# Performance work log

Measured on AMD Instinct MI355X. Metric: run time of the kernel, lower is better.

The kernel has to match this reference:

```python
import jax, jax.numpy as jnp
import numpy as np

B, C, H, W = 16, 256, 32, 32
NUM_LAYERS = 30
OUT = 16  # sqrt(out_channels)
EPS = 1e-5


def setup_inputs() -> dict:
    key = jax.random.key(0)
    k1, k2, k3 = jax.random.split(key, 3)
    x = jax.random.normal(k1, (B, C, H, W), dtype=jnp.float32)
    # delta_t ~ small positive values (module inits ~N(0.01, 0.005))
    delta_t = jax.random.uniform(k2, (NUM_LAYERS, 1), dtype=jnp.float32) * 0.02
    matrices = jax.random.normal(k3, (NUM_LAYERS, 1, 1, OUT, OUT), dtype=jnp.float32) * 0.1
    gamma = jnp.ones((H * W,), dtype=jnp.float32)   # BatchNorm2d weight, oc = i*i = H*W
    beta = jnp.zeros((H * W,), dtype=jnp.float32)   # BatchNorm2d bias
    return {"x": x, "delta_t": delta_t, "matrices": matrices, "gamma": gamma, "beta": beta}


def _bn_relu6(z, gamma, beta):
    # training-mode BatchNorm2d over channel axis 1 (channels = H*W), then ReLU6
    mean = jnp.mean(z, axis=(0, 2, 3), keepdims=True)
    var = jnp.mean(jnp.square(z - mean), axis=(0, 2, 3), keepdims=True)  # biased var
    zhat = (z - mean) * jax.lax.rsqrt(var + EPS)
    g = gamma.reshape(1, -1, 1, 1)
    b = beta.reshape(1, -1, 1, 1)
    return jnp.clip(zhat * g + b, 0.0, 6.0)


def reference(x, delta_t, matrices, gamma, beta):
    b, c, h, w = x.shape
    hw = h * w
    # feature_reshape: [B,C,H,W] -> [B,HW,C] -> [B,HW,out,out] (inn == out branch)
    x1 = x.reshape(b, c, hw).transpose(0, 2, 1).reshape(b, hw, OUT, OUT)
    dt = jnp.clip(delta_t, 0.0, 6.0)[:, 0]  # relu6(delta_t), shape [L]

    def step(y0, params):
        m, dtl = params  # m: [1,1,out,out] broadcasts elementwise against x1
        dydt = -y0 + _bn_relu6(y0 + m * x1, gamma, beta)
        return y0 + dtl * dydt, None

    y0, _ = jax.lax.scan(step, x1, (matrices, dt))
    # (y0 + x1): [B, HW, out, out] -> view [B,H,W,out*out] -> permute to [B,out*out,H,W]
    y = (y0 + x1).reshape(b, h, w, OUT * OUT).transpose(0, 3, 1, 2)
    return y
```

## Files before the change

kernel.cpp:

```cpp
#include <hip/hip_runtime.h>

typedef float v2f __attribute__((ext_vector_type(2)));
typedef float v4f __attribute__((ext_vector_type(4)));

#define HW      1024
#define NROWS   4096
#define NLAYERS 30
#define TPB     256

static __device__ __forceinline__ v2f pk_fma(v2f a, v2f b, v2f c) {
    v2f d; asm("v_pk_fma_f32 %0, %1, %2, %3" : "=v"(d) : "v"(a), "v"(b), "v"(c));
    return d;
}
static __device__ __forceinline__ v2f pk_add(v2f a, v2f b) {
    v2f d; asm("v_pk_add_f32 %0, %1, %2" : "=v"(d) : "v"(a), "v"(b));
    return d;
}
static __device__ __forceinline__ v2f pk_mul(v2f a, v2f b) {
    v2f d; asm("v_pk_mul_f32 %0, %1, %2" : "=v"(d) : "v"(a), "v"(b));
    return d;
}

template <int CTRL, int RMASK>
__device__ __forceinline__ float dpp_add(float x) {
    int t = __builtin_amdgcn_update_dpp(0, __builtin_bit_cast(int, x),
                                        CTRL, RMASK, 0xf, true);
    return x + __builtin_bit_cast(float, t);
}
__device__ __forceinline__ float wave_sum64(float x) {
    x = dpp_add<0x111, 0xf>(x);
    x = dpp_add<0x112, 0xf>(x);
    x = dpp_add<0x114, 0xf>(x);
    x = dpp_add<0x118, 0xf>(x);
    x = dpp_add<0x142, 0xa>(x);
    x = dpp_add<0x143, 0xc>(x);
    return x;
}
__device__ __forceinline__ float bcast63(float x) {
    return __builtin_bit_cast(float,
        __builtin_amdgcn_readlane(__builtin_bit_cast(int, x), 63));
}

__global__ __launch_bounds__(TPB) void txp64(const float* __restrict__ src,
                                             float* __restrict__ dst,
                                             int M, int N) {
    __shared__ float tile[64][65];
    const int n0 = blockIdx.x * 64;
    const int m0 = blockIdx.y * 64;
    const int tx = threadIdx.x & 63;
    const int ty = threadIdx.x >> 6;
#pragma unroll
    for (int i = 0; i < 16; ++i) {
        const int r = ty + 4 * i;
        tile[r][tx] = src[(size_t)(m0 + r) * N + n0 + tx];
    }
    __syncthreads();
#pragma unroll
    for (int i = 0; i < 16; ++i) {
        const int r = ty + 4 * i;
        dst[(size_t)(n0 + r) * M + m0 + tx] = tile[tx][r];
    }
}

__global__ __launch_bounds__(64, 1) void ode_zrec(
    float* ws, const float* __restrict__ delta_t,
    const float* __restrict__ matrices, const float* __restrict__ gamma,
    const float* __restrict__ beta) {

    const int p    = blockIdx.x;
    const int lane = threadIdx.x;
    const int c0   = 4 * lane;
    float* row = ws + (size_t)p * NROWS;

    __shared__ float xs[NROWS];

    const float gp = gamma[p];
    const float bp = beta[p];

    v2f z[32];
    v2f s0 = {0.f, 0.f}, s1 = {0.f, 0.f}, q0 = {0.f, 0.f}, q1 = {0.f, 0.f};

    {
        const v4f m4 = *(const v4f*)(matrices + c0);
        const v2f mA = {m4.x, m4.y}, mB = {m4.z, m4.w};
#pragma unroll
        for (int j = 0; j < 16; ++j) {
            const v4f x4 = *(const v4f*)(row + 4 * lane + 256 * j);
            *(v4f*)&xs[4 * lane + 256 * j] = x4;
            const v2f xA = {x4.x, x4.y}, xB = {x4.z, x4.w};
            z[2 * j]     = pk_fma(mA, xA, xA);
            z[2 * j + 1] = pk_fma(mB, xB, xB);
            s0 = pk_add(s0, z[2 * j]);
            q0 = pk_fma(z[2 * j], z[2 * j], q0);
            s1 = pk_add(s1, z[2 * j + 1]);
            q1 = pk_fma(z[2 * j + 1], z[2 * j + 1], q1);
        }
    }

    v4f   mqc = *(const v4f*)(matrices + c0);
    v4f   mqn = *(const v4f*)(matrices + 256 + c0);
    float dtc = delta_t[0];
    float dtn = delta_t[1];

    for (int k = 0; k < NLAYERS - 1; ++k) {
        const int k2 = (k + 2 < NLAYERS) ? k + 2 : NLAYERS - 1;
        const v4f   mq2   = *(const v4f*)(matrices + k2 * 256 + c0);
        const float dt_nn = delta_t[k2];

        const v2f sv = pk_add(s0, s1);
        const v2f qv = pk_add(q0, q1);
        const float S = bcast63(wave_sum64(sv.x + sv.y));
        const float Q = bcast63(wave_sum64(qv.x + qv.y));

        const float dtk  = __builtin_amdgcn_fmed3f(dtc, 0.0f, 6.0f);
        const float mean = S * (1.0f / 4096.0f);
        const float var  = fmaf(-mean, mean, Q * (1.0f / 4096.0f));
        const float rstd = rsqrtf(var + 1e-5f);
        const float g    = gp * rstd;
        const float b    = fmaf(-mean, g, bp);
        const float om   = 1.0f - dtk;
        const v2f g2 = {g, g}, b2 = {b, b};
        const v2f dt2 = {dtk, dtk};
        const v2f om2 = {om, om};
        const v2f omn = {-om, -om};
        const v2f mcA = {mqc.x, mqc.y}, mcB = {mqc.z, mqc.w};
        const v2f mnA = {mqn.x, mqn.y}, mnB = {mqn.z, mqn.w};
        const v2f dmA = pk_fma(omn, mcA, mnA);
        const v2f dmB = pk_fma(omn, mcB, mnB);

        s0 = (v2f){0.f, 0.f}; s1 = (v2f){0.f, 0.f};
        q0 = (v2f){0.f, 0.f}; q1 = (v2f){0.f, 0.f};

#pragma unroll
        for (int j = 0; j < 16; ++j) {
            const v4f x4 = *(const v4f*)&xs[4 * lane + 256 * j];
            const v2f xA = {x4.x, x4.y}, xB = {x4.z, x4.w};
            {
                const int e = 2 * j;
                v2f a = pk_fma(z[e], g2, b2);
                a.x = __builtin_amdgcn_fmed3f(a.x, 0.0f, 6.0f);
                a.y = __builtin_amdgcn_fmed3f(a.y, 0.0f, 6.0f);
                v2f t = pk_mul(dt2, a);
                t = pk_fma(dmA, xA, t);
                z[e] = pk_fma(om2, z[e], t);
                s0 = pk_add(s0, z[e]);
                q0 = pk_fma(z[e], z[e], q0);
            }
            {
                const int e = 2 * j + 1;
                v2f a = pk_fma(z[e], g2, b2);
                a.x = __builtin_amdgcn_fmed3f(a.x, 0.0f, 6.0f);
                a.y = __builtin_amdgcn_fmed3f(a.y, 0.0f, 6.0f);
                v2f t = pk_mul(dt2, a);
                t = pk_fma(dmB, xB, t);
                z[e] = pk_fma(om2, z[e], t);
                s1 = pk_add(s1, z[e]);
                q1 = pk_fma(z[e], z[e], q1);
            }
        }

        mqc = mqn; mqn = mq2; dtc = dtn; dtn = dt_nn;
    }

    {
        const v2f sv = pk_add(s0, s1);
        const v2f qv = pk_add(q0, q1);
        const float S = bcast63(wave_sum64(sv.x + sv.y));
        const float Q = bcast63(wave_sum64(qv.x + qv.y));

        const float dtk  = __builtin_amdgcn_fmed3f(dtc, 0.0f, 6.0f);
        const float mean = S * (1.0f / 4096.0f);
        const float var  = fmaf(-mean, mean, Q * (1.0f / 4096.0f));
        const float rstd = rsqrtf(var + 1e-5f);
        const float g    = gp * rstd;
        const float b    = fmaf(-mean, g, bp);
        const float om   = 1.0f - dtk;
        const v2f g2 = {g, g}, b2 = {b, b};
        const v2f dt2 = {dtk, dtk};
        const v2f om2 = {om, om};
        const v2f omn = {-om, -om};
        const v2f one2 = {1.0f, 1.0f};
        const v2f mcA = {mqc.x, mqc.y}, mcB = {mqc.z, mqc.w};
        const v2f dmA = pk_fma(omn, mcA, one2);
        const v2f dmB = pk_fma(omn, mcB, one2);

#pragma unroll
        for (int j = 0; j < 16; ++j) {
            const v4f x4 = *(const v4f*)&xs[4 * lane + 256 * j];
            const v2f xA = {x4.x, x4.y}, xB = {x4.z, x4.w};
            v2f o0, o1;
            {
                const int e = 2 * j;
                v2f a = pk_fma(z[e], g2, b2);
                a.x = __builtin_amdgcn_fmed3f(a.x, 0.0f, 6.0f);
                a.y = __builtin_amdgcn_fmed3f(a.y, 0.0f, 6.0f);
                v2f t = pk_mul(dt2, a);
                t = pk_fma(dmA, xA, t);
                o0 = pk_fma(om2, z[e], t);
            }
            {
                const int e = 2 * j + 1;
                v2f a = pk_fma(z[e], g2, b2);
                a.x = __builtin_amdgcn_fmed3f(a.x, 0.0f, 6.0f);
                a.y = __builtin_amdgcn_fmed3f(a.y, 0.0f, 6.0f);
                v2f t = pk_mul(dt2, a);
                t = pk_fma(dmB, xB, t);
                o1 = pk_fma(om2, z[e], t);
            }
            v4f o4; o4.x = o0.x; o4.y = o0.y; o4.z = o1.x; o4.w = o1.y;
            *(v4f*)(row + 4 * lane + 256 * j) = o4;
        }
    }
}

__global__ __launch_bounds__(TPB) void ode_fused(const float* __restrict__ x,
                                                 const float* __restrict__ delta_t,
                                                 const float* __restrict__ matrices,
                                                 const float* __restrict__ gamma,
                                                 const float* __restrict__ beta,
                                                 float* __restrict__ out) {
    const int bid = blockIdx.x;
    const int p   = ((bid & 7) << 7) | (bid >> 3);
    const int t   = threadIdx.x;

    __shared__ float smat[(NLAYERS + 1) * 256];
    __shared__ float sdt[NLAYERS];
    __shared__ __align__(16) v2f red[2][4];

#pragma unroll
    for (int i = 0; i < NLAYERS; ++i)
        smat[i * 256 + t] = matrices[i * 256 + t];
    if (t < NLAYERS)
        sdt[t] = __builtin_amdgcn_fmed3f(delta_t[t], 0.0f, 6.0f);

    v2f x1[8], y[8];
#pragma unroll
    for (int k = 0; k < 8; ++k) {
        x1[k].x = x[(size_t)(t + 512 * k) * HW + p];
        x1[k].y = x[(size_t)(t + 512 * k + 256) * HW + p];
        y[k] = x1[k];
    }

    const float gp   = gamma[p];
    const float bp   = beta[p];
    const int   wid  = t >> 6;
    const int   lane = t & 63;

    __syncthreads();
    float m_cur = smat[t];

    for (int l = 0; l < NLAYERS; ++l) {
        const float dtl = sdt[l];
        const v2f m2    = {m_cur, m_cur};
        const v2f dt2   = {dtl, dtl};
        const v2f om2   = {1.0f - dtl, 1.0f - dtl};

        v2f z[8];
        v2f sA = {0.f, 0.f}, sB = {0.f, 0.f};
        v2f qA = {0.f, 0.f}, qB = {0.f, 0.f};
#pragma unroll
        for (int k = 0; k < 8; k += 2) {
            z[k]     = __builtin_elementwise_fma(m2, x1[k], y[k]);
            z[k + 1] = __builtin_elementwise_fma(m2, x1[k + 1], y[k + 1]);
            sA += z[k];
            sB += z[k + 1];
            qA = __builtin_elementwise_fma(z[k], z[k], qA);
            qB = __builtin_elementwise_fma(z[k + 1], z[k + 1], qB);
        }
#pragma unroll
        for (int k = 0; k < 8; ++k) y[k] *= om2;

        const v2f sv = sA + sB;
        const v2f qv = qA + qB;
        float s = wave_sum64(sv.x + sv.y);
        float q = wave_sum64(qv.x + qv.y);

        const int par = l & 1;
        if (lane == 63) { v2f w; w.x = s; w.y = q; red[par][wid] = w; }
        m_cur = smat[(l + 1) * 256 + t];
        __syncthreads();

        const float4 r0 = *(const float4*)&red[par][0];
        const float4 r1 = *(const float4*)&red[par][2];
        const float S  = (r0.x + r0.z) + (r1.x + r1.z);
        const float S2 = (r0.y + r0.w) + (r1.y + r1.w);

        const float mean = S * (1.0f / 4096.0f);
        const float var  = fmaf(-mean, mean, S2 * (1.0f / 4096.0f));
        const float rstd = rsqrtf(var + 1e-5f);
        const float g    = gp * rstd;
        const float bb   = fmaf(-mean, g, bp);
        const v2f g2 = {g, g}, b2 = {bb, bb};
        const v2f z0 = {0.f, 0.f}, s6 = {6.f, 6.f};
#pragma unroll
        for (int k = 0; k < 8; ++k) {
            v2f a = __builtin_elementwise_fma(z[k], g2, b2);
            a = __builtin_elementwise_max(a, z0);
            a = __builtin_elementwise_min(a, s6);
            y[k] = __builtin_elementwise_fma(dt2, a, y[k]);
        }
    }

#pragma unroll
    for (int k = 0; k < 8; ++k) {
        out[(size_t)(t + 512 * k) * HW + p]       = y[k].x + x1[k].x;
        out[(size_t)(t + 512 * k + 256) * HW + p] = y[k].y + x1[k].y;
    }
}

extern "C" void kernel_launch(void* const* d_in, const int* in_sizes, int n_in,
                              void* d_out, int out_size, void* d_ws, size_t ws_size,
                              hipStream_t stream) {
    const float* x        = (const float*)d_in[0];
    const float* delta_t  = (const float*)d_in[1];
    const float* matrices = (const float*)d_in[2];
    const float* gamma    = (const float*)d_in[3];
    const float* beta     = (const float*)d_in[4];
    float* out = (float*)d_out;

    const size_t need = (size_t)HW * NROWS * sizeof(float);
    if (d_ws != nullptr && ws_size >= need) {
        float* ws = (float*)d_ws;
        txp64<<<dim3(HW / 64, NROWS / 64), dim3(TPB), 0, stream>>>(x, ws, NROWS, HW);
        ode_zrec<<<dim3(HW), dim3(64), 0, stream>>>(ws, delta_t, matrices, gamma, beta);
        txp64<<<dim3(NROWS / 64, HW / 64), dim3(TPB), 0, stream>>>(ws, out, HW, NROWS);
    } else {
        ode_fused<<<dim3(HW), dim3(TPB), 0, stream>>>(x, delta_t, matrices, gamma, beta, out);
    }
}
```

Measured before the change: 119.1 us.

## Split per-channel ODE recurrence across four waves with LDS double-buffered reduction

The per-channel recurrence kernel now uses 256 threads (four waves) per channel instead of one wave, so each thread holds 8 packed registers rather than 32. The BN statistics become a cross-wave reduction through a double-buffered shared array with one barrier per layer. The dt scaling is also folded into the gain, bias and clamp bound, which drops one packed multiply per element. This trades a per-layer block barrier and LDS traffic for more parallelism, shorter per-thread serial chains and better latency hiding.

```diff
diff --git a/kernel.cpp b/kernel.cpp
--- a/kernel.cpp
+++ b/kernel.cpp
@@ -14,10 +14,6 @@
 }
 static __device__ __forceinline__ v2f pk_add(v2f a, v2f b) {
     v2f d; asm("v_pk_add_f32 %0, %1, %2" : "=v"(d) : "v"(a), "v"(b));
-    return d;
-}
-static __device__ __forceinline__ v2f pk_mul(v2f a, v2f b) {
-    v2f d; asm("v_pk_mul_f32 %0, %1, %2" : "=v"(d) : "v"(a), "v"(b));
     return d;
 }
 
@@ -36,10 +32,6 @@
     x = dpp_add<0x143, 0xc>(x);
     return x;
 }
-__device__ __forceinline__ float bcast63(float x) {
-    return __builtin_bit_cast(float,
-        __builtin_amdgcn_readlane(__builtin_bit_cast(int, x), 63));
-}
 
 __global__ __launch_bounds__(TPB) void txp64(const float* __restrict__ src,
                                              float* __restrict__ dst,
@@ -62,31 +54,34 @@
     }
 }
 
-__global__ __launch_bounds__(64, 1) void ode_zrec(
+__global__ __launch_bounds__(TPB, 4) void ode_z4w(
     float* ws, const float* __restrict__ delta_t,
     const float* __restrict__ matrices, const float* __restrict__ gamma,
     const float* __restrict__ beta) {
 
     const int p    = blockIdx.x;
-    const int lane = threadIdx.x;
-    const int c0   = 4 * lane;
+    const int t    = threadIdx.x;
+    const int wid  = t >> 6;
+    const int lane = t & 63;
+    const int c0   = (4 * t) & 255;
     float* row = ws + (size_t)p * NROWS;
 
     __shared__ float xs[NROWS];
+    __shared__ __align__(16) v2f red[2][4];
 
     const float gp = gamma[p];
     const float bp = beta[p];
 
-    v2f z[32];
+    v2f z[8];
     v2f s0 = {0.f, 0.f}, s1 = {0.f, 0.f}, q0 = {0.f, 0.f}, q1 = {0.f, 0.f};
 
     {
         const v4f m4 = *(const v4f*)(matrices + c0);
         const v2f mA = {m4.x, m4.y}, mB = {m4.z, m4.w};
 #pragma unroll
-        for (int j = 0; j < 16; ++j) {
-            const v4f x4 = *(const v4f*)(row + 4 * lane + 256 * j);
-            *(v4f*)&xs[4 * lane + 256 * j] = x4;
+        for (int j = 0; j < 4; ++j) {
+            const v4f x4 = *(const v4f*)(row + 4 * t + 1024 * j);
+            *(v4f*)&xs[4 * t + 1024 * j] = x4;
             const v2f xA = {x4.x, x4.y}, xB = {x4.z, x4.w};
             z[2 * j]     = pk_fma(mA, xA, xA);
             z[2 * j + 1] = pk_fma(mB, xB, xB);
@@ -95,22 +90,29 @@
             s1 = pk_add(s1, z[2 * j + 1]);
             q1 = pk_fma(z[2 * j + 1], z[2 * j + 1], q1);
         }
+        const v2f sv = pk_add(s0, s1);
+        const v2f qv = pk_add(q0, q1);
+        const float ss = wave_sum64(sv.x + sv.y);
+        const float qq = wave_sum64(qv.x + qv.y);
+        if (lane == 63) red[0][wid] = (v2f){ss, qq};
     }
 
     v4f   mqc = *(const v4f*)(matrices + c0);
     v4f   mqn = *(const v4f*)(matrices + 256 + c0);
     float dtc = delta_t[0];
     float dtn = delta_t[1];
+    __syncthreads();
 
     for (int k = 0; k < NLAYERS - 1; ++k) {
         const int k2 = (k + 2 < NLAYERS) ? k + 2 : NLAYERS - 1;
         const v4f   mq2   = *(const v4f*)(matrices + k2 * 256 + c0);
         const float dt_nn = delta_t[k2];
 
-        const v2f sv = pk_add(s0, s1);
-        const v2f qv = pk_add(q0, q1);
-        const float S = bcast63(wave_sum64(sv.x + sv.y));
-        const float Q = bcast63(wave_sum64(qv.x + qv.y));
+        const int par = k & 1;
+        const v4f r0 = *(const v4f*)&red[par][0];
+        const v4f r1 = *(const v4f*)&red[par][2];
+        const float S = (r0.x + r0.z) + (r1.x + r1.z);
+        const float Q = (r0.y + r0.w) + (r1.y + r1.w);
 
         const float dtk  = __builtin_amdgcn_fmed3f(dtc, 0.0f, 6.0f);
         const float mean = S * (1.0f / 4096.0f);
@@ -119,8 +121,10 @@
         const float g    = gp * rstd;
         const float b    = fmaf(-mean, g, bp);
         const float om   = 1.0f - dtk;
-        const v2f g2 = {g, g}, b2 = {b, b};
-        const v2f dt2 = {dtk, dtk};
+        const float gd   = g * dtk;
+        const float bd   = b * dtk;
+        const float hi   = 6.0f * dtk;
+        const v2f gd2 = {gd, gd}, bd2 = {bd, bd};
         const v2f om2 = {om, om};
         const v2f omn = {-om, -om};
         const v2f mcA = {mqc.x, mqc.y}, mcB = {mqc.z, mqc.w};
@@ -132,41 +136,45 @@
         q0 = (v2f){0.f, 0.f}; q1 = (v2f){0.f, 0.f};
 
 #pragma unroll
-        for (int j = 0; j < 16; ++j) {
-            const v4f x4 = *(const v4f*)&xs[4 * lane + 256 * j];
+        for (int j = 0; j < 4; ++j) {
+            const v4f x4 = *(const v4f*)&xs[4 * t + 1024 * j];
             const v2f xA = {x4.x, x4.y}, xB = {x4.z, x4.w};
             {
                 const int e = 2 * j;
-                v2f a = pk_fma(z[e], g2, b2);
-                a.x = __builtin_amdgcn_fmed3f(a.x, 0.0f, 6.0f);
-                a.y = __builtin_amdgcn_fmed3f(a.y, 0.0f, 6.0f);
-                v2f t = pk_mul(dt2, a);
-                t = pk_fma(dmA, xA, t);
-                z[e] = pk_fma(om2, z[e], t);
+                v2f a = pk_fma(z[e], gd2, bd2);
+                a.x = __builtin_amdgcn_fmed3f(a.x, 0.0f, hi);
+                a.y = __builtin_amdgcn_fmed3f(a.y, 0.0f, hi);
+                v2f u = pk_fma(dmA, xA, a);
+                z[e] = pk_fma(om2, z[e], u);
                 s0 = pk_add(s0, z[e]);
                 q0 = pk_fma(z[e], z[e], q0);
             }
             {
                 const int e = 2 * j + 1;
-                v2f a = pk_fma(z[e], g2, b2);
-                a.x = __builtin_amdgcn_fmed3f(a.x, 0.0f, 6.0f);
-                a.y = __builtin_amdgcn_fmed3f(a.y, 0.0f, 6.0f);
-                v2f t = pk_mul(dt2, a);
-                t = pk_fma(dmB, xB, t);
-                z[e] = pk_fma(om2, z[e], t);
+                v2f a = pk_fma(z[e], gd2, bd2);
+                a.x = __builtin_amdgcn_fmed3f(a.x, 0.0f, hi);
+                a.y = __builtin_amdgcn_fmed3f(a.y, 0.0f, hi);
+                v2f u = pk_fma(dmB, xB, a);
+                z[e] = pk_fma(om2, z[e], u);
                 s1 = pk_add(s1, z[e]);
                 q1 = pk_fma(z[e], z[e], q1);
             }
         }
-
-        mqc = mqn; mqn = mq2; dtc = dtn; dtn = dt_nn;
-    }
-
-    {
         const v2f sv = pk_add(s0, s1);
         const v2f qv = pk_add(q0, q1);
-        const float S = bcast63(wave_sum64(sv.x + sv.y));
-        const float Q = bcast63(wave_sum64(qv.x + qv.y));
+        const float ss = wave_sum64(sv.x + sv.y);
+        const float qq = wave_sum64(qv.x + qv.y);
+        if (lane == 63) red[par ^ 1][wid] = (v2f){ss, qq};
+
+        mqc = mqn; mqn = mq2; dtc = dtn; dtn = dt_nn;
+        __syncthreads();
+    }
+
+    {
+        const v4f r0 = *(const v4f*)&red[(NLAYERS - 1) & 1][0];
+        const v4f r1 = *(const v4f*)&red[(NLAYERS - 1) & 1][2];
+        const float S = (r0.x + r0.z) + (r1.x + r1.z);
+        const float Q = (r0.y + r0.w) + (r1.y + r1.w);
 
         const float dtk  = __builtin_amdgcn_fmed3f(dtc, 0.0f, 6.0f);
         const float mean = S * (1.0f / 4096.0f);
@@ -175,8 +183,10 @@
         const float g    = gp * rstd;
         const float b    = fmaf(-mean, g, bp);
         const float om   = 1.0f - dtk;
-        const v2f g2 = {g, g}, b2 = {b, b};
-        const v2f dt2 = {dtk, dtk};
+        const float gd   = g * dtk;
+        const float bd   = b * dtk;
+        const float hi   = 6.0f * dtk;
+        const v2f gd2 = {gd, gd}, bd2 = {bd, bd};
         const v2f om2 = {om, om};
         const v2f omn = {-om, -om};
         const v2f one2 = {1.0f, 1.0f};
@@ -185,30 +195,28 @@
         const v2f dmB = pk_fma(omn, mcB, one2);
 
 #pragma unroll
-        for (int j = 0; j < 16; ++j) {
-            const v4f x4 = *(const v4f*)&xs[4 * lane + 256 * j];
+        for (int j = 0; j < 4; ++j) {
+            const v4f x4 = *(const v4f*)&xs[4 * t + 1024 * j];
             const v2f xA = {x4.x, x4.y}, xB = {x4.z, x4.w};
             v2f o0, o1;
             {
                 const int e = 2 * j;
-                v2f a = pk_fma(z[e], g2, b2);
-                a.x = __builtin_amdgcn_fmed3f(a.x, 0.0f, 6.0f);
-                a.y = __builtin_amdgcn_fmed3f(a.y, 0.0f, 6.0f);
-                v2f t = pk_mul(dt2, a);
-                t = pk_fma(dmA, xA, t);
-                o0 = pk_fma(om2, z[e], t);
+                v2f a = pk_fma(z[e], gd2, bd2);
+                a.x = __builtin_amdgcn_fmed3f(a.x, 0.0f, hi);
+                a.y = __builtin_amdgcn_fmed3f(a.y, 0.0f, hi);
+                v2f u = pk_fma(dmA, xA, a);
+                o0 = pk_fma(om2, z[e], u);
             }
             {
                 const int e = 2 * j + 1;
-                v2f a = pk_fma(z[e], g2, b2);
-                a.x = __builtin_amdgcn_fmed3f(a.x, 0.0f, 6.0f);
-                a.y = __builtin_amdgcn_fmed3f(a.y, 0.0f, 6.0f);
-                v2f t = pk_mul(dt2, a);
-                t = pk_fma(dmB, xB, t);
-                o1 = pk_fma(om2, z[e], t);
+                v2f a = pk_fma(z[e], gd2, bd2);
+                a.x = __builtin_amdgcn_fmed3f(a.x, 0.0f, hi);
+                a.y = __builtin_amdgcn_fmed3f(a.y, 0.0f, hi);
+                v2f u = pk_fma(dmB, xB, a);
+                o1 = pk_fma(om2, z[e], u);
             }
             v4f o4; o4.x = o0.x; o4.y = o0.y; o4.z = o1.x; o4.w = o1.y;
-            *(v4f*)(row + 4 * lane + 256 * j) = o4;
+            *(v4f*)(row + 4 * t + 1024 * j) = o4;
         }
     }
 }
@@ -322,7 +330,7 @@
     if (d_ws != nullptr && ws_size >= need) {
         float* ws = (float*)d_ws;
         txp64<<<dim3(HW / 64, NROWS / 64), dim3(TPB), 0, stream>>>(x, ws, NROWS, HW);
-        ode_zrec<<<dim3(HW), dim3(64), 0, stream>>>(ws, delta_t, matrices, gamma, beta);
+        ode_z4w<<<dim3(HW), dim3(TPB), 0, stream>>>(ws, delta_t, matrices, gamma, beta);
         txp64<<<dim3(NROWS / 64, HW / 64), dim3(TPB), 0, stream>>>(ws, out, HW, NROWS);
     } else {
         ode_fused<<<dim3(HW), dim3(TPB), 0, stream>>>(x, delta_t, matrices, gamma, beta, out);
```

After: 119.7 us. About the same (+0.5%).
